# Kernel tuning notes

Measured on AMD Instinct MI355X. Metric: run time of the kernel, lower is better.

## Reference

```python
import jax, jax.numpy as jnp
import numpy as np

D = 256        # embedding_dim
K = 4096       # num_embeddings
DECAY = 0.99
EPS = 1e-05
COMMIT = 0.25


def setup_inputs() -> dict:
    key = jax.random.key(0)
    kx, ke = jax.random.split(key)
    x = jax.random.normal(kx, (32, 1024, D), dtype=jnp.float32)
    # variance_scaling(scale=1.0, mode='fan_in', distribution='uniform') on (D, K): fan_in = D
    limit = np.sqrt(3.0 / D).astype(np.float32)
    embeddings = jax.random.uniform(ke, (D, K), dtype=jnp.float32, minval=-limit, maxval=limit)
    return {
        'x': x,
        'embeddings': embeddings,
        'ema_counter': jnp.zeros((), jnp.float32),
        'ema_hidden_cluster': jnp.zeros((K,), jnp.float32),
        'ema_hidden_dw': jnp.zeros((D, K), jnp.float32),
    }


def reference(x, embeddings, ema_counter, ema_hidden_cluster, ema_hidden_dw):
    flat = x.reshape(-1, D)  # [N, D]
    # squared euclidean distance to each code: [N, K]
    distance = (jnp.sum(flat ** 2, axis=1, keepdims=True)
                - 2.0 * jnp.matmul(flat, embeddings)
                + jnp.sum(embeddings ** 2, axis=0, keepdims=True))
    encoding_indices = jnp.argmax(-distance, axis=1)           # [N]
    encodings = jax.nn.one_hot(encoding_indices, K, dtype=distance.dtype)  # [N, K]
    idx = encoding_indices.reshape(x.shape[:-1])               # [B, T]
    quantized = jnp.take(embeddings.T, idx, axis=0)            # [B, T, D]

    e_latent_loss = jnp.mean((quantized - x) ** 2)
    q_latent_loss = jnp.mean((quantized - x) ** 2)
    vq_loss = q_latent_loss + COMMIT * e_latent_loss

    # EMA codebook update (training=True path); debiased EMA per the module
    counter = ema_counter + 1.0
    bias = 1.0 - jnp.power(DECAY, counter)
    cluster_hidden = ema_hidden_cluster * DECAY + jnp.sum(encodings, axis=0) * (1.0 - DECAY)
    cluster_avg = cluster_hidden / bias                         # [K]
    dw = jnp.matmul(flat.T, encodings)                          # [D, K]
    dw_hidden = ema_hidden_dw * DECAY + dw * (1.0 - DECAY)
    dw_avg = dw_hidden / bias                                   # [D, K]
    n = jnp.sum(cluster_avg)
    cluster_norm = (cluster_avg + EPS) / (n + K * EPS) * n
    new_embeddings = dw_avg / cluster_norm[None, :]             # [D, K]

    avg_probs = jnp.mean(encodings, axis=0)
    perplexity = jnp.exp(-jnp.sum(avg_probs * jnp.log(avg_probs + 1e-10)))
    return quantized, vq_loss, perplexity, idx, new_embeddings
```

## Files before the change

### kernel.cpp

```cpp
#include <hip/hip_runtime.h>
#include <math.h>

#define N_TOK 32768
#define DIM   256
#define KCODE 4096

#define WS_E2      0
#define WS_COUNTS  4096
#define WS_LOSSP   8192
#define WS_SCAL    8448
#define WS_CNORM   8512
#define WS_IDX     12608
#define WS_EHS     307520
#define WS_DWT     1356096
#define WS_CARRYV  2404672
#define WS_CARRYI  2437440
#define WS_OFFS    2470208
#define WS_WOFF    2474304

#define OUT_Q      0
#define OUT_LOSS   8388608
#define OUT_PERP   8388609
#define OUT_IDX    8388610
#define OUT_EMB    8421378

#define EH_PLANE   1048576
#define XH_PLANE   8388608

typedef _Float16 f16x8 __attribute__((ext_vector_type(8)));
typedef _Float16 f16x4 __attribute__((ext_vector_type(4)));
typedef float    f32x4 __attribute__((ext_vector_type(4)));

__global__ void k_e2(const float* __restrict__ emb, float* __restrict__ e2)
{
    int k  = blockIdx.x * 256 + threadIdx.x;
    int d0 = blockIdx.y * 32;
    float s = 0.0f;
#pragma unroll 8
    for (int d = 0; d < 32; ++d) {
        float v = emb[(size_t)(d0 + d) * KCODE + k];
        s += v * v;
    }
    atomicAdd(&e2[k], s);
}

__global__ void k_split_x(const float* __restrict__ x, unsigned short* __restrict__ xh)
{
    int i = (blockIdx.x * 256 + threadIdx.x) * 8;
    float4 f0 = *(const float4*)(x + i);
    float4 f1 = *(const float4*)(x + i + 4);
    float fv[8] = {f0.x, f0.y, f0.z, f0.w, f1.x, f1.y, f1.z, f1.w};
    f16x8 h1, h2;
#pragma unroll
    for (int j = 0; j < 8; ++j) {
        _Float16 a = (_Float16)fv[j];
        h1[j] = a;
        h2[j] = (_Float16)(fv[j] - (float)a);
    }
    *(f16x8*)((_Float16*)xh + i)            = h1;
    *(f16x8*)((_Float16*)xh + XH_PLANE + i) = h2;
}

__global__ void k_split_e(const float* __restrict__ emb, unsigned short* __restrict__ ehs_)
{
    __shared__ float tile[32][33];
    _Float16* ehs = (_Float16*)ehs_;
    int t  = threadIdx.x;
    int tx = t & 31, iy = t >> 5;
    int k0 = blockIdx.x * 32, d0 = blockIdx.y * 32;
#pragma unroll
    for (int j = 0; j < 4; ++j)
        tile[iy + 8 * j][tx] = emb[(size_t)(d0 + iy + 8 * j) * KCODE + k0 + tx];
    __syncthreads();
    int code = k0 + tx;
    size_t base = (size_t)(((code >> 8) * 8) + (d0 >> 5)) * 8192 + (code & 255) * 32 + iy * 4;
    f16x4 h1, h2;
#pragma unroll
    for (int j = 0; j < 4; ++j) {
        float v = tile[iy * 4 + j][tx];
        _Float16 a = (_Float16)v;
        h1[j] = a;
        h2[j] = (_Float16)(v - (float)a);
    }
    *(f16x4*)(ehs + base)            = h1;
    *(f16x4*)(ehs + EH_PLANE + base) = h2;
}

__global__ __launch_bounds__(256, 2)
void k_argmin(const unsigned short* __restrict__ xh_, const unsigned short* __restrict__ ehs_,
              const float* __restrict__ e2, int* __restrict__ idx_out,
              float* __restrict__ carryV, int* __restrict__ carryI,
              float* __restrict__ out_idxf, float* __restrict__ counts,
              int ct0, int phase)
{
    __shared__ __align__(16) _Float16 Ah[2][64][256];

    const _Float16* xh  = (const _Float16*)xh_;
    const _Float16* ehs = (const _Float16*)ehs_;

    const int t    = threadIdx.x;
    const int lane = t & 63, w = t >> 6;
    const int lo   = lane & 15, q = lane >> 4;
    const int row0 = blockIdx.x * 64;

    {
        int m = t >> 3, kb = (t & 7) * 32;
#pragma unroll
        for (int p = 0; p < 2; ++p)
#pragma unroll
            for (int rr = 0; rr < 2; ++rr) {
                int mm = m + 32 * rr;
                const _Float16* src = xh + (size_t)p * XH_PLANE + (size_t)(row0 + mm) * DIM + kb;
#pragma unroll
                for (int g = 0; g < 4; ++g) {
                    f16x8 h = __builtin_nontemporal_load((const f16x8*)(src + g * 8));
                    int grp = ((kb >> 3) + g) ^ (mm & 7);
                    *(f16x8*)&Ah[p][mm][grp * 8] = h;
                }
            }
    }
    __syncthreads();

    float best[16];
    int   bidx[16];
#pragma unroll
    for (int s = 0; s < 16; ++s) { best[s] = 3.4e38f; bidx[s] = 0; }

    const _Float16* ehp1 = ehs + (size_t)(w * 64 + lo) * 32 + q * 8;
    const _Float16* ehp2 = ehp1 + EH_PLANE;

    f16x8 b1f[2][4], b2f[2][4];
    {
        const size_t so0 = (size_t)(ct0 * 8) * 8192;
#pragma unroll
        for (int nf = 0; nf < 4; ++nf) {
            b1f[0][nf] = *(const f16x8*)(ehp1 + so0 + nf * 512);
            b2f[0][nf] = *(const f16x8*)(ehp2 + so0 + nf * 512);
        }
    }

    for (int ct = ct0; ct < ct0 + 8; ++ct) {
        f32x4 acc[4][4];
#pragma unroll
        for (int mf = 0; mf < 4; ++mf)
#pragma unroll
            for (int nf = 0; nf < 4; ++nf) acc[mf][nf] = (f32x4)0.0f;

#pragma unroll
        for (int ks = 0; ks < 8; ++ks) {
            const int cur = ks & 1, nxt = cur ^ 1;
            const int so  = ct * 8 + ks;

            if (ks < 7 || ct < ct0 + 7) {
                const size_t po = (size_t)(so + 1) * 8192;
#pragma unroll
                for (int nf = 0; nf < 4; ++nf) {
                    b1f[nxt][nf] = *(const f16x8*)(ehp1 + po + nf * 512);
                    b2f[nxt][nf] = *(const f16x8*)(ehp2 + po + nf * 512);
                }
            }
            __builtin_amdgcn_sched_barrier(0);

            const int agrp = ((ks * 4 + q) ^ (lo & 7)) * 8;
            f16x8 a1[4], a2[4];
#pragma unroll
            for (int mf = 0; mf < 4; ++mf)
                a2[mf] = *(const f16x8*)&Ah[1][mf * 16 + lo][agrp];
#pragma unroll
            for (int mf = 0; mf < 4; ++mf)
                a1[mf] = *(const f16x8*)&Ah[0][mf * 16 + lo][agrp];

            __builtin_amdgcn_s_setprio(1);
#pragma unroll
            for (int nf = 0; nf < 4; ++nf) {
#pragma unroll
                for (int mf = 0; mf < 4; ++mf) {
                    acc[mf][nf] = __builtin_amdgcn_mfma_f32_16x16x32_f16(a2[mf], b1f[cur][nf], acc[mf][nf], 0, 0, 0);
                    acc[mf][nf] = __builtin_amdgcn_mfma_f32_16x16x32_f16(a1[mf], b2f[cur][nf], acc[mf][nf], 0, 0, 0);
                    acc[mf][nf] = __builtin_amdgcn_mfma_f32_16x16x32_f16(a1[mf], b1f[cur][nf], acc[mf][nf], 0, 0, 0);
                }
            }
            __builtin_amdgcn_s_setprio(0);
        }

#pragma unroll
        for (int nf = 0; nf < 4; ++nf) {
            int cl = w * 64 + nf * 16 + lo;
            float e2v = e2[ct * 256 + cl];
#pragma unroll
            for (int mf = 0; mf < 4; ++mf)
#pragma unroll
                for (int r = 0; r < 4; ++r) {
                    float dist = fmaf(-2.0f, acc[mf][nf][r], e2v);
                    int s = mf * 4 + r;
                    if (dist < best[s]) { best[s] = dist; bidx[s] = ct * 256 + cl; }
                }
        }
    }

    __syncthreads();
    float* rv = (float*)&Ah[0][0][0];
    int*   ri = (int*)(((char*)&Ah[0][0][0]) + 16384);
#pragma unroll
    for (int s = 0; s < 16; ++s) {
        int row = (s >> 2) * 16 + q * 4 + (s & 3);
        rv[row * 64 + w * 16 + lo] = best[s];
        ri[row * 64 + w * 16 + lo] = bidx[s];
    }
    __syncthreads();
    if (t < 64) {
        float bv; int bi;
        if (phase) { bv = carryV[row0 + t]; bi = carryI[row0 + t]; }
        else       { bv = 3.4e38f; bi = 0x40000000; }
        for (int jj = 0; jj < 64; ++jj) {
            int j = (jj + t) & 63;
            float v = rv[t * 64 + j];
            int  ii = ri[t * 64 + j];
            if (v < bv || (v == bv && ii < bi)) { bv = v; bi = ii; }
        }
        if (phase) {
            idx_out[row0 + t] = bi;
            out_idxf[row0 + t] = (float)bi;
            atomicAdd(&counts[bi], 1.0f);
        } else {
            carryV[row0 + t] = bv; carryI[row0 + t] = bi;
        }
    }
}

__global__ void k_scan(const float* __restrict__ counts, int* __restrict__ offs,
                       int* __restrict__ woff)
{
    __shared__ int ps[256];
    int t = threadIdx.x;
    int local[16];
    int s = 0;
#pragma unroll
    for (int j = 0; j < 16; ++j) {
        local[j] = s;
        s += (int)counts[t * 16 + j];
    }
    ps[t] = s;
    __syncthreads();
    for (int off = 1; off < 256; off <<= 1) {
        int v = (t >= off) ? ps[t - off] : 0;
        __syncthreads();
        ps[t] += v;
        __syncthreads();
    }
    int base = (t > 0) ? ps[t - 1] : 0;
#pragma unroll
    for (int j = 0; j < 16; ++j) {
        int o = base + local[j];
        offs[t * 16 + j] = o;
        woff[t * 16 + j] = o;
    }
}

__global__ void k_scatter(const int* __restrict__ idx, int* __restrict__ woff,
                          int* __restrict__ rowlist)
{
    int n = blockIdx.x * 256 + threadIdx.x;
    int k = idx[n];
    int pos = atomicAdd(&woff[k], 1);
    rowlist[pos] = n;
}

__global__ void k_dw(const float* __restrict__ x, const int* __restrict__ rowlist,
                     const int* __restrict__ offs, const float* __restrict__ counts,
                     float* __restrict__ dwT)
{
    __shared__ float red[4][256];
    int k = blockIdx.x;
    int t = threadIdx.x;
    int lane = t & 63, w = t >> 6;
    int start = offs[k];
    int cnt   = (int)counts[k];
    float4 acc = {0.0f, 0.0f, 0.0f, 0.0f};
    int j = w;
    for (; j + 4 < cnt; j += 8) {
        int n0 = rowlist[start + j];
        int n1 = rowlist[start + j + 4];
        float4 v0 = *(const float4*)&x[(size_t)n0 * DIM + lane * 4];
        float4 v1 = *(const float4*)&x[(size_t)n1 * DIM + lane * 4];
        acc.x += v0.x + v1.x; acc.y += v0.y + v1.y;
        acc.z += v0.z + v1.z; acc.w += v0.w + v1.w;
    }
    if (j < cnt) {
        int n0 = rowlist[start + j];
        float4 v0 = *(const float4*)&x[(size_t)n0 * DIM + lane * 4];
        acc.x += v0.x; acc.y += v0.y; acc.z += v0.z; acc.w += v0.w;
    }
    *(float4*)&red[w][lane * 4] = acc;
    __syncthreads();
    float s = red[0][t] + red[1][t] + red[2][t] + red[3][t];
    dwT[(size_t)k * DIM + t] = s;
}

__global__ void k_gather(const float* __restrict__ x, const unsigned short* __restrict__ ehs_,
                         const int* __restrict__ idx, float* __restrict__ out_q,
                         float* __restrict__ lossp)
{
    const _Float16* ehs = (const _Float16*)ehs_;
    int t = threadIdx.x;
    int lane = t & 63, w = t >> 6;
    int n = blockIdx.x * 4 + w;
    int k = idx[n];
    float4 xv = *(const float4*)&x[(size_t)n * DIM + lane * 4];
    size_t base = (size_t)(((k >> 8) * 8) + (lane >> 3)) * 8192 + (k & 255) * 32 + (lane & 7) * 4;
    f16x4 h1 = *(const f16x4*)(ehs + base);
    f16x4 h2 = *(const f16x4*)(ehs + EH_PLANE + base);
    float4 ev;
    ev.x = (float)h1[0] + (float)h2[0];
    ev.y = (float)h1[1] + (float)h2[1];
    ev.z = (float)h1[2] + (float)h2[2];
    ev.w = (float)h1[3] + (float)h2[3];
    *(float4*)&out_q[(size_t)n * DIM + lane * 4] = ev;
    float dx = ev.x - xv.x, dy = ev.y - xv.y, dz = ev.z - xv.z, dw = ev.w - xv.w;
    float s = dx * dx + dy * dy + dz * dz + dw * dw;
#pragma unroll
    for (int off = 32; off > 0; off >>= 1) s += __shfl_down(s, off, 64);
    if (lane == 0) atomicAdd(&lossp[blockIdx.x & 255], s);
}

__global__ void k_finalize(const float* __restrict__ counts, const float* __restrict__ lossp,
                           const float* __restrict__ ema_counter,
                           const float* __restrict__ ema_cluster,
                           float* __restrict__ cnorm, float* __restrict__ scal,
                           float* __restrict__ out)
{
    __shared__ float red[256];
    int t = threadIdx.x;
    float ls = lossp[t];
    float ent = 0.0f, casum = 0.0f;
    float ca[16];
#pragma unroll
    for (int j = 0; j < 16; ++j) {
        int k = j * 256 + t;
        float c = counts[k];
        float p = c * (1.0f / 32768.0f);
        ent += p * logf(p + 1e-10f);
        ca[j] = ema_cluster[k] * 0.99f + c * 0.01f;
        casum += ca[j];
    }
    red[t] = ls; __syncthreads();
    for (int o = 128; o > 0; o >>= 1) { if (t < o) red[t] += red[t + o]; __syncthreads(); }
    float loss_tot = red[0]; __syncthreads();
    red[t] = ent; __syncthreads();
    for (int o = 128; o > 0; o >>= 1) { if (t < o) red[t] += red[t + o]; __syncthreads(); }
    float ent_tot = red[0]; __syncthreads();
    red[t] = casum; __syncthreads();
    for (int o = 128; o > 0; o >>= 1) { if (t < o) red[t] += red[t + o]; __syncthreads(); }
    float casum_tot = red[0]; __syncthreads();

    float bias = 1.0f - powf(0.99f, ema_counter[0] + 1.0f);
    float n = casum_tot / bias;
    float inv = n / (n + 4096.0f * 1e-5f);
#pragma unroll
    for (int j = 0; j < 16; ++j) {
        int k = j * 256 + t;
        cnorm[k] = (ca[j] / bias + 1e-5f) * inv;
    }
    if (t == 0) {
        out[OUT_LOSS] = 1.25f * loss_tot * (1.0f / (32768.0f * 256.0f));
        out[OUT_PERP] = expf(-ent_tot);
        scal[0] = bias;
    }
}

__global__ void k_newemb(const float* __restrict__ dwT, const float* __restrict__ ema_dw,
                         const float* __restrict__ cnorm, const float* __restrict__ scal,
                         float* __restrict__ out_emb)
{
    __shared__ float tile[32][33];
    int t = threadIdx.x;
    int tx = t & 31, iy = t >> 5;
    int k0 = blockIdx.x * 32, d0 = blockIdx.y * 32;
#pragma unroll
    for (int j = 0; j < 4; ++j)
        tile[iy + 8 * j][tx] = dwT[(size_t)(k0 + iy + 8 * j) * DIM + d0 + tx];
    __syncthreads();
    float inv_bias = 1.0f / scal[0];
    float cn = cnorm[k0 + tx];
#pragma unroll
    for (int j = 0; j < 4; ++j) {
        int d = d0 + iy + 8 * j;
        float dwv = tile[tx][iy + 8 * j];
        float hid = ema_dw[(size_t)d * KCODE + k0 + tx] * 0.99f + dwv * 0.01f;
        out_emb[(size_t)d * KCODE + k0 + tx] = hid * inv_bias / cn;
    }
}

extern "C" void kernel_launch(void* const* d_in, const int* in_sizes, int n_in,
                              void* d_out, int out_size, void* d_ws, size_t ws_size,
                              hipStream_t stream)
{
    const float* x           = (const float*)d_in[0];
    const float* emb         = (const float*)d_in[1];
    const float* ema_counter = (const float*)d_in[2];
    const float* ema_cluster = (const float*)d_in[3];
    const float* ema_dw      = (const float*)d_in[4];
    float* out = (float*)d_out;
    float* ws  = (float*)d_ws;

    float* e2     = ws + WS_E2;
    float* counts = ws + WS_COUNTS;
    float* lossp  = ws + WS_LOSSP;
    float* scal   = ws + WS_SCAL;
    float* cnorm  = ws + WS_CNORM;
    int*   idxw   = (int*)(ws + WS_IDX);
    unsigned short* ehs = (unsigned short*)(ws + WS_EHS);
    float* dwT    = ws + WS_DWT;
    float* carryV = ws + WS_CARRYV;
    int*   carryI = (int*)(ws + WS_CARRYI);
    int*   rowlist= (int*)(ws + WS_CARRYV);
    int*   offs   = (int*)(ws + WS_OFFS);
    int*   woff   = (int*)(ws + WS_WOFF);
    unsigned short* xh = (unsigned short*)(out + OUT_Q);

    hipMemsetAsync(e2, 0, (size_t)WS_CNORM * sizeof(float), stream);

    k_e2<<<dim3(16, 8), 256, 0, stream>>>(emb, e2);
    k_split_e<<<dim3(128, 8), 256, 0, stream>>>(emb, ehs);
    k_split_x<<<4096, 256, 0, stream>>>(x, xh);
    k_argmin<<<512, 256, 0, stream>>>(xh, ehs, e2, idxw, carryV, carryI,
                                      out + OUT_IDX, counts, 0, 0);
    k_argmin<<<512, 256, 0, stream>>>(xh, ehs, e2, idxw, carryV, carryI,
                                      out + OUT_IDX, counts, 8, 1);
    k_gather<<<8192, 256, 0, stream>>>(x, ehs, idxw, out + OUT_Q, lossp);
    k_scan<<<1, 256, 0, stream>>>(counts, offs, woff);
    k_scatter<<<128, 256, 0, stream>>>(idxw, woff, rowlist);
    k_dw<<<4096, 256, 0, stream>>>(x, rowlist, offs, counts, dwT);
    k_finalize<<<1, 256, 0, stream>>>(counts, lossp, ema_counter, ema_cluster,
                                      cnorm, scal, out);
    k_newemb<<<dim3(128, 8), 256, 0, stream>>>(dwT, ema_dw, cnorm, scal, out + OUT_EMB);
}
```

Before: 363.3 us.

## Halve argmin row tile to 32 and drop B-fragment register prefetch for occupancy

The argmin GEMM kernel now handles 32 token rows per block instead of 64, which halves the shared-memory A tile and the accumulator and best/index registers. It launches twice as many blocks and raises launch bounds to 4 blocks per CU. The double-buffered register prefetch of codebook fragments is replaced by plain loads each k-step, and the MFMAs are regrouped by pass. The goal is higher occupancy to hide latency, at the cost of each B fragment being reused across half as many rows, so global/L2 traffic for the codebook doubles and the explicit prefetch overlap is lost.

```diff
diff --git a/kernel.cpp b/kernel.cpp
--- a/kernel.cpp
+++ b/kernel.cpp
@@ -86,14 +86,14 @@
     *(f16x4*)(ehs + EH_PLANE + base) = h2;
 }
 
-__global__ __launch_bounds__(256, 2)
+__global__ __launch_bounds__(256, 4)
 void k_argmin(const unsigned short* __restrict__ xh_, const unsigned short* __restrict__ ehs_,
               const float* __restrict__ e2, int* __restrict__ idx_out,
               float* __restrict__ carryV, int* __restrict__ carryI,
               float* __restrict__ out_idxf, float* __restrict__ counts,
               int ct0, int phase)
 {
-    __shared__ __align__(16) _Float16 Ah[2][64][256];
+    __shared__ __align__(16) _Float16 Ah[2][32][256];
 
     const _Float16* xh  = (const _Float16*)xh_;
     const _Float16* ehs = (const _Float16*)ehs_;
@@ -101,85 +101,73 @@
     const int t    = threadIdx.x;
     const int lane = t & 63, w = t >> 6;
     const int lo   = lane & 15, q = lane >> 4;
-    const int row0 = blockIdx.x * 64;
+    const int row0 = blockIdx.x * 32;
 
     {
         int m = t >> 3, kb = (t & 7) * 32;
 #pragma unroll
-        for (int p = 0; p < 2; ++p)
-#pragma unroll
-            for (int rr = 0; rr < 2; ++rr) {
-                int mm = m + 32 * rr;
-                const _Float16* src = xh + (size_t)p * XH_PLANE + (size_t)(row0 + mm) * DIM + kb;
-#pragma unroll
-                for (int g = 0; g < 4; ++g) {
-                    f16x8 h = __builtin_nontemporal_load((const f16x8*)(src + g * 8));
-                    int grp = ((kb >> 3) + g) ^ (mm & 7);
-                    *(f16x8*)&Ah[p][mm][grp * 8] = h;
-                }
+        for (int p = 0; p < 2; ++p) {
+            const _Float16* src = xh + (size_t)p * XH_PLANE + (size_t)(row0 + m) * DIM + kb;
+#pragma unroll
+            for (int g = 0; g < 4; ++g) {
+                f16x8 h = __builtin_nontemporal_load((const f16x8*)(src + g * 8));
+                int grp = ((kb >> 3) + g) ^ (m & 7);
+                *(f16x8*)&Ah[p][m][grp * 8] = h;
             }
-    }
-    __syncthreads();
-
-    float best[16];
-    int   bidx[16];
-#pragma unroll
-    for (int s = 0; s < 16; ++s) { best[s] = 3.4e38f; bidx[s] = 0; }
+        }
+    }
+    __syncthreads();
+
+    float best[8];
+    int   bidx[8];
+#pragma unroll
+    for (int s = 0; s < 8; ++s) { best[s] = 3.4e38f; bidx[s] = 0; }
 
     const _Float16* ehp1 = ehs + (size_t)(w * 64 + lo) * 32 + q * 8;
     const _Float16* ehp2 = ehp1 + EH_PLANE;
 
-    f16x8 b1f[2][4], b2f[2][4];
-    {
-        const size_t so0 = (size_t)(ct0 * 8) * 8192;
-#pragma unroll
-        for (int nf = 0; nf < 4; ++nf) {
-            b1f[0][nf] = *(const f16x8*)(ehp1 + so0 + nf * 512);
-            b2f[0][nf] = *(const f16x8*)(ehp2 + so0 + nf * 512);
-        }
-    }
-
     for (int ct = ct0; ct < ct0 + 8; ++ct) {
-        f32x4 acc[4][4];
-#pragma unroll
-        for (int mf = 0; mf < 4; ++mf)
+        f32x4 acc[2][4];
+#pragma unroll
+        for (int mf = 0; mf < 2; ++mf)
 #pragma unroll
             for (int nf = 0; nf < 4; ++nf) acc[mf][nf] = (f32x4)0.0f;
 
 #pragma unroll
         for (int ks = 0; ks < 8; ++ks) {
-            const int cur = ks & 1, nxt = cur ^ 1;
-            const int so  = ct * 8 + ks;
-
-            if (ks < 7 || ct < ct0 + 7) {
-                const size_t po = (size_t)(so + 1) * 8192;
-#pragma unroll
-                for (int nf = 0; nf < 4; ++nf) {
-                    b1f[nxt][nf] = *(const f16x8*)(ehp1 + po + nf * 512);
-                    b2f[nxt][nf] = *(const f16x8*)(ehp2 + po + nf * 512);
-                }
+            const size_t so = (size_t)(ct * 8 + ks) * 8192;
+
+            f16x8 b1[4], b2[4];
+#pragma unroll
+            for (int nf = 0; nf < 4; ++nf) {
+                b1[nf] = *(const f16x8*)(ehp1 + so + nf * 512);
+                b2[nf] = *(const f16x8*)(ehp2 + so + nf * 512);
             }
-            __builtin_amdgcn_sched_barrier(0);
 
             const int agrp = ((ks * 4 + q) ^ (lo & 7)) * 8;
-            f16x8 a1[4], a2[4];
-#pragma unroll
-            for (int mf = 0; mf < 4; ++mf)
+            f16x8 a1[2], a2[2];
+#pragma unroll
+            for (int mf = 0; mf < 2; ++mf) {
                 a2[mf] = *(const f16x8*)&Ah[1][mf * 16 + lo][agrp];
-#pragma unroll
-            for (int mf = 0; mf < 4; ++mf)
                 a1[mf] = *(const f16x8*)&Ah[0][mf * 16 + lo][agrp];
+            }
 
             __builtin_amdgcn_s_setprio(1);
 #pragma unroll
-            for (int nf = 0; nf < 4; ++nf) {
-#pragma unroll
-                for (int mf = 0; mf < 4; ++mf) {
-                    acc[mf][nf] = __builtin_amdgcn_mfma_f32_16x16x32_f16(a2[mf], b1f[cur][nf], acc[mf][nf], 0, 0, 0);
-                    acc[mf][nf] = __builtin_amdgcn_mfma_f32_16x16x32_f16(a1[mf], b2f[cur][nf], acc[mf][nf], 0, 0, 0);
-                    acc[mf][nf] = __builtin_amdgcn_mfma_f32_16x16x32_f16(a1[mf], b1f[cur][nf], acc[mf][nf], 0, 0, 0);
-                }
-            }
+            for (int nf = 0; nf < 4; ++nf)
+#pragma unroll
+                for (int mf = 0; mf < 2; ++mf)
+                    acc[mf][nf] = __builtin_amdgcn_mfma_f32_16x16x32_f16(a2[mf], b1[nf], acc[mf][nf], 0, 0, 0);
+#pragma unroll
+            for (int nf = 0; nf < 4; ++nf)
+#pragma unroll
+                for (int mf = 0; mf < 2; ++mf)
+                    acc[mf][nf] = __builtin_amdgcn_mfma_f32_16x16x32_f16(a1[mf], b2[nf], acc[mf][nf], 0, 0, 0);
+#pragma unroll
+            for (int nf = 0; nf < 4; ++nf)
+#pragma unroll
+                for (int mf = 0; mf < 2; ++mf)
+                    acc[mf][nf] = __builtin_amdgcn_mfma_f32_16x16x32_f16(a1[mf], b1[nf], acc[mf][nf], 0, 0, 0);
             __builtin_amdgcn_s_setprio(0);
         }
 
@@ -188,7 +176,7 @@
             int cl = w * 64 + nf * 16 + lo;
             float e2v = e2[ct * 256 + cl];
 #pragma unroll
-            for (int mf = 0; mf < 4; ++mf)
+            for (int mf = 0; mf < 2; ++mf)
 #pragma unroll
                 for (int r = 0; r < 4; ++r) {
                     float dist = fmaf(-2.0f, acc[mf][nf][r], e2v);
@@ -200,15 +188,15 @@
 
     __syncthreads();
     float* rv = (float*)&Ah[0][0][0];
-    int*   ri = (int*)(((char*)&Ah[0][0][0]) + 16384);
-#pragma unroll
-    for (int s = 0; s < 16; ++s) {
+    int*   ri = (int*)(((char*)&Ah[0][0][0]) + 8192);
+#pragma unroll
+    for (int s = 0; s < 8; ++s) {
         int row = (s >> 2) * 16 + q * 4 + (s & 3);
         rv[row * 64 + w * 16 + lo] = best[s];
         ri[row * 64 + w * 16 + lo] = bidx[s];
     }
     __syncthreads();
-    if (t < 64) {
+    if (t < 32) {
         float bv; int bi;
         if (phase) { bv = carryV[row0 + t]; bi = carryI[row0 + t]; }
         else       { bv = 3.4e38f; bi = 0x40000000; }
@@ -423,10 +411,10 @@
     k_e2<<<dim3(16, 8), 256, 0, stream>>>(emb, e2);
     k_split_e<<<dim3(128, 8), 256, 0, stream>>>(emb, ehs);
     k_split_x<<<4096, 256, 0, stream>>>(x, xh);
-    k_argmin<<<512, 256, 0, stream>>>(xh, ehs, e2, idxw, carryV, carryI,
-                                      out + OUT_IDX, counts, 0, 0);
-    k_argmin<<<512, 256, 0, stream>>>(xh, ehs, e2, idxw, carryV, carryI,
-                                      out + OUT_IDX, counts, 8, 1);
+    k_argmin<<<1024, 256, 0, stream>>>(xh, ehs, e2, idxw, carryV, carryI,
+                                       out + OUT_IDX, counts, 0, 0);
+    k_argmin<<<1024, 256, 0, stream>>>(xh, ehs, e2, idxw, carryV, carryI,
+                                       out + OUT_IDX, counts, 8, 1);
     k_gather<<<8192, 256, 0, stream>>>(x, ehs, idxw, out + OUT_Q, lossp);
     k_scan<<<1, 256, 0, stream>>>(counts, offs, woff);
     k_scatter<<<128, 256, 0, stream>>>(idxw, woff, rowlist);
```

After: 650.9 us. +79.1%, slower.
